# Kernel tuning notes

Hardware: AMD Instinct MI355X
Metric: run time of the kernel (lower is better)

The kernel has to match this reference:

```python
import jax, jax.numpy as jnp
import numpy as np

WINDOW, SIM_TH, GAMMA, L_MAX, NUM_HEADS = 32, 0.7, 0.8, 1024, 8


def setup_inputs() -> dict:
    key = jax.random.key(0)
    ks = jax.random.split(key, 12)
    B, N, F, D, S, V, C = 8, 16384, 1024, 512, 64, 30522, 4
    padded_bags = jax.random.normal(ks[0], (B, N, F), jnp.float32)
    lengths = jax.random.randint(ks[1], (B,), N // 4, N + 1)
    key_padding_mask = jnp.arange(N)[None, :] >= lengths[:, None]  # True = pad (tail)
    input_ids = jax.random.randint(ks[2], (B, S), 0, V)
    attention_mask = jnp.ones((B, S), jnp.int32)

    def xav(k, shape):
        lim = np.sqrt(6.0 / (shape[0] + shape[1]))
        return jax.random.uniform(k, shape, jnp.float32, -lim, lim)

    emb_table = jax.random.normal(ks[3], (V, 768), jnp.float32) * 0.02
    return dict(
        padded_bags=padded_bags, key_padding_mask=key_padding_mask,
        input_ids=input_ids, attention_mask=attention_mask,
        emb_table=emb_table,
        W_tp=xav(ks[4], (768, D)), b_tp=jnp.zeros((D,), jnp.float32),
        W_enc=xav(ks[5], (F, D)), b_enc=jnp.zeros((D,), jnp.float32),
        ln_g=jnp.ones((D,), jnp.float32), ln_b=jnp.zeros((D,), jnp.float32),
        Wq=xav(ks[6], (D, D)), bq=jnp.zeros((D,), jnp.float32),
        Wk=xav(ks[7], (D, D)), bk=jnp.zeros((D,), jnp.float32),
        Wv=xav(ks[8], (D, D)), bv=jnp.zeros((D,), jnp.float32),
        Wo=xav(ks[9], (D, D)), bo=jnp.zeros((D,), jnp.float32),
        W_cls=xav(ks[10], (D, C)), b_cls=jnp.zeros((C,), jnp.float32),
    )


def reference(padded_bags, key_padding_mask, input_ids, attention_mask,
              emb_table, W_tp, b_tp, W_enc, b_enc, ln_g, ln_b,
              Wq, bq, Wk, bk, Wv, bv, Wo, bo, W_cls, b_cls):
    B, N, _ = padded_bags.shape
    D = W_enc.shape[1]
    # --- frozen text encoder surrogate (DistilBERT is frozen + no_grad in original):
    # token embedding + masked mean pooling stands in for the CLS feature [B,768]
    tok = emb_table[input_ids]                                   # [B,S,768]
    am = attention_mask[..., None].astype(jnp.float32)
    text_feat = (tok * am).sum(1) / jnp.maximum(am.sum(1), 1.0)
    text_feat = jax.lax.stop_gradient(text_feat)
    text_emb = text_feat @ W_tp + b_tp                           # [B,D]
    # --- feature encoder: Linear + LayerNorm + ReLU (dropout = eval identity) ---
    h = padded_bags @ W_enc + b_enc                              # [B,N,D]
    mu = h.mean(-1, keepdims=True)
    var = ((h - mu) ** 2).mean(-1, keepdims=True)
    img = jax.nn.relu(ln_g * (h - mu) / jnp.sqrt(var + 1e-5) + ln_b)
    valid = ~key_padding_mask                                    # [B,N]
    # --- Stage 1: sliding-window (size 32) cosine-similarity redundancy pruning ---
    fn = img / (jnp.linalg.norm(img, axis=-1, keepdims=True) + 1e-8)
    neg = jnp.full((B, N), -jnp.inf, jnp.float32)
    max_sim = neg
    for w in range(1, WINDOW + 1):                               # fixed small window loop
        sim_w = (fn[:, w:] * fn[:, :-w]).sum(-1)                 # [B,N-w]
        sim_w = jnp.where(valid[:, :-w], sim_w, -jnp.inf)
        max_sim = jnp.maximum(max_sim, jnp.concatenate([neg[:, :w], sim_w], axis=1))
    keep1 = valid & (max_sim < SIM_TH)                           # [B,N]
    # --- Stage 2: language-guided top-k by text relevance, kept in original order ---
    rel = jnp.einsum('bnd,bd->bn', img, text_emb)
    rel_m = jnp.where(keep1, rel, -jnp.inf)
    n_kept = keep1.sum(-1)
    k_b = jnp.clip((GAMMA * n_kept.astype(jnp.float32)).astype(jnp.int32), 1, L_MAX)
    _, idx = jax.lax.top_k(rel_m, L_MAX)                         # [B,L_MAX]
    sel = jnp.arange(L_MAX)[None, :] < k_b[:, None]
    idx_sorted = jnp.sort(jnp.where(sel, idx, N), axis=-1)       # sort -> original order
    mask2 = idx_sorted < N
    feat2 = jnp.take_along_axis(img, jnp.clip(idx_sorted, 0, N - 1)[..., None], axis=1)
    feat2 = jnp.where(mask2[..., None], feat2, 0.0)              # [B,L_MAX,D] zero-repadded
    # --- Stage 3: sequential visual token compression (adjacent-pair mean pooling) ---
    M = L_MAX // 2
    f2 = feat2.reshape(B, M, 2, D)
    pm = mask2.reshape(B, M, 2).astype(jnp.float32)
    feat3 = (f2 * pm[..., None]).sum(2) / jnp.maximum(pm.sum(2), 1.0)[..., None]  # [B,M,D]
    # --- cross-modal MHA aggregator (text query; zero-padded keys DO attend, as in original) ---
    H = NUM_HEADS
    dh = D // H
    q = (text_emb @ Wq + bq).reshape(B, H, dh)
    k = (feat3 @ Wk + bk).reshape(B, M, H, dh)
    v = (feat3 @ Wv + bv).reshape(B, M, H, dh)
    scores = jnp.einsum('bhd,bmhd->bhm', q, k) / np.float32(np.sqrt(dh))
    attn = jax.nn.softmax(scores, axis=-1)
    ctx = jnp.einsum('bhm,bmhd->bhd', attn, v).reshape(B, D)
    out = ctx @ Wo + bo
    return out @ W_cls + b_cls                                   # [B,num_classes]
```

## Files before the change

kernel.cpp:

```cpp
#include <hip/hip_runtime.h>
#include <hip/hip_bf16.h>
#include <math.h>
#include <stdint.h>

#define B_    8
#define N_    16384
#define F_    1024
#define D_    512
#define S_    64
#define H_    8
#define DH_   64
#define LMAX_ 1024
#define M2_   512
#define WIN_  32
#define NTOK_ (B_ * N_)

typedef __attribute__((ext_vector_type(8)))  short bf16x8;
typedef __attribute__((ext_vector_type(16))) float f32x16;

#define S_OF(r) (((r) >> 1) & 3)

static __device__ __forceinline__ float wred_sum(float v) {
    #pragma unroll
    for (int d = 1; d < 64; d <<= 1) v += __shfl_xor(v, d, 64);
    return v;
}

static __device__ __forceinline__ void bf8_to_f32(uint4 q, float* a) {
    a[0] = __uint_as_float(q.x << 16); a[1] = __uint_as_float(q.x & 0xffff0000u);
    a[2] = __uint_as_float(q.y << 16); a[3] = __uint_as_float(q.y & 0xffff0000u);
    a[4] = __uint_as_float(q.z << 16); a[5] = __uint_as_float(q.z & 0xffff0000u);
    a[6] = __uint_as_float(q.w << 16); a[7] = __uint_as_float(q.w & 0xffff0000u);
}

static __device__ __forceinline__ unsigned short bf16r(float x) {
    unsigned int b = __float_as_uint(x);
    return (unsigned short)((b + 0x7FFFu + ((b >> 16) & 1u)) >> 16);
}

static __device__ __forceinline__ void split_bf(float x, unsigned short& h, unsigned short& l) {
    unsigned int b = __float_as_uint(x);
    unsigned int hb = (b + 0x7FFFu + ((b >> 16) & 1u)) >> 16;
    h = (unsigned short)hb;
    float r = x - __uint_as_float(hb << 16);
    l = bf16r(r);
}

static __device__ __forceinline__ void split8(float4 f0, float4 f1, bf16x8& hi, bf16x8& lo) {
    float xs[8] = { f0.x, f0.y, f0.z, f0.w, f1.x, f1.y, f1.z, f1.w };
    unsigned int hp[4], lp[4];
    #pragma unroll
    for (int i = 0; i < 4; i++) {
        unsigned int b0 = __float_as_uint(xs[2*i]), b1 = __float_as_uint(xs[2*i+1]);
        hp[i] = (b0 >> 16) | (b1 & 0xffff0000u);
        float r0 = xs[2*i]   - __uint_as_float(b0 & 0xffff0000u);
        float r1 = xs[2*i+1] - __uint_as_float(b1 & 0xffff0000u);
        lp[i] = (__float_as_uint(r0) >> 16) | (__float_as_uint(r1) & 0xffff0000u);
    }
    union { uint4 u; bf16x8 v; } a, c;
    a.u = make_uint4(hp[0], hp[1], hp[2], hp[3]);
    c.u = make_uint4(lp[0], lp[1], lp[2], lp[3]);
    hi = a.v; lo = c.v;
}

static __device__ __forceinline__ void gll16(const void* g, void* l) {
    __builtin_amdgcn_global_load_lds(
        (const __attribute__((address_space(1))) unsigned int*)g,
        (__attribute__((address_space(3))) unsigned int*)l, 16, 0, 0);
}

__global__ void k_detect(const unsigned char* mb, int nbytes, int* flag) {
    int found = 0;
    for (int i = blockIdx.x * blockDim.x + threadIdx.x; i < nbytes; i += gridDim.x * blockDim.x)
        if ((i & 3) && mb[i]) found = 1;
    if (found) atomicOr(flag, 1);
}

__global__ void k_valid(const void* maskp, const int* flag, unsigned char* v) {
    int i = blockIdx.x * 256 + threadIdx.x;
    if (i >= NTOK_) return;
    int pad;
    if (*flag) pad = (((const unsigned char*)maskp)[i] != 0);
    else       pad = (((const int*)maskp)[i] != 0);
    v[i] = pad ? 0 : 1;
}

__global__ void k_text_feat(const float* emb, const int* ids, const int* am, float* tf) {
    int b = blockIdx.x;
    __shared__ int   sid[S_];
    __shared__ float sam[S_];
    int t = threadIdx.x;
    if (t < S_) { sid[t] = ids[b * S_ + t]; sam[t] = (float)am[b * S_ + t]; }
    __syncthreads();
    float asum = 0.f;
    for (int s = 0; s < S_; s++) asum += sam[s];
    float denom = fmaxf(asum, 1.0f);
    for (int d = t; d < 768; d += blockDim.x) {
        float acc = 0.f;
        for (int s = 0; s < S_; s++) acc += emb[(long)sid[s] * 768 + d] * sam[s];
        tf[b * 768 + d] = acc / denom;
    }
}

__global__ void k_rowmm(const float* in, const float* W, const float* bias,
                        float* out, int E, int Nn) {
    int b = blockIdx.x, d = threadIdx.x;
    __shared__ float sin[768];
    for (int e = d; e < E; e += blockDim.x) sin[e] = in[b * E + e];
    __syncthreads();
    float acc = bias[d];
    for (int e = 0; e < E; e++) acc = fmaf(sin[e], W[(long)e * Nn + d], acc);
    out[b * Nn + d] = acc;
}

__global__ __launch_bounds__(256) void k_bsplit_sw(const float* __restrict__ W,
                                                   unsigned short* __restrict__ bh,
                                                   unsigned short* __restrict__ bl,
                                                   int E) {
    __shared__ float tile[32][33];
    int e0 = blockIdx.x * 32;
    int d0 = blockIdx.y * 32;
    int t = threadIdx.x;
    int r = t >> 3, c4 = (t & 7) * 4;
    float4 v = *(const float4*)(W + (long)(e0 + r) * D_ + d0 + c4);
    tile[r][c4] = v.x; tile[r][c4 + 1] = v.y; tile[r][c4 + 2] = v.z; tile[r][c4 + 3] = v.w;
    __syncthreads();
    if (t < 128) {
        int c = t & 31, kq = t >> 5;
        int col = d0 + c;
        float xs[8];
        #pragma unroll
        for (int i = 0; i < 8; i++) xs[i] = tile[kq * 8 + i][c];
        unsigned short h[8], l[8];
        #pragma unroll
        for (int i = 0; i < 8; i++) split_bf(xs[i], h[i], l[i]);
        uint4 ph, pl;
        ph.x = h[0] | ((unsigned)h[1] << 16); ph.y = h[2] | ((unsigned)h[3] << 16);
        ph.z = h[4] | ((unsigned)h[5] << 16); ph.w = h[6] | ((unsigned)h[7] << 16);
        pl.x = l[0] | ((unsigned)l[1] << 16); pl.y = l[2] | ((unsigned)l[3] << 16);
        pl.z = l[4] | ((unsigned)l[5] << 16); pl.w = l[6] | ((unsigned)l[7] << 16);
        int Q = (e0 >> 3) + kq;
        int Qo = (Q & ~3) | ((Q & 3) ^ S_OF(col & 7));
        *(uint4*)(bh + (long)col * E + Qo * 8) = ph;
        *(uint4*)(bl + (long)col * E + Qo * 8) = pl;
    }
}

static __device__ __forceinline__ void gemm3_body(const float* __restrict__ A,
                                                  const unsigned short* __restrict__ Bh2,
                                                  const unsigned short* __restrict__ Bl2,
                                                  const float* __restrict__ bias,
                                                  float* __restrict__ C, int K, int wg) {
    __shared__ __align__(16) float ldsA[128][32];
    __shared__ __align__(16) unsigned short ldsB[2][128][32];
    int bn = wg & 3, bm = wg >> 2;
    int tid = threadIdx.x;
    int w = tid >> 6, lane = tid & 63;
    int r32 = lane & 31, kg = lane >> 5;
    int wr = w >> 1, wc = w & 1;
    int s8 = r32 & 7;

    const float* agbase = nullptr;
    const unsigned short* bgbase = nullptr;
    if (w < 2) {
        int rl = lane >> 3, qs = lane & 7;
        agbase = A + (long)(bm * 128 + w * 64 + rl) * K + ((qs ^ rl) * 4);
    } else {
        const unsigned short* plane = (w == 2) ? Bh2 : Bl2;
        int lrow = lane >> 2, lq = lane & 3;
        bgbase = plane + (long)(bn * 128 + lrow) * K + lq * 8;
    }

    f32x16 acc[2][2];
    #pragma unroll
    for (int i = 0; i < 2; i++)
        #pragma unroll
        for (int j = 0; j < 2; j++)
            #pragma unroll
            for (int r = 0; r < 16; r++) acc[i][j][r] = 0.f;

    for (int kt = 0; kt < K; kt += 32) {
        if (w < 2) {
            #pragma unroll
            for (int j = 0; j < 8; j++)
                gll16(agbase + (long)j * 8 * K + kt, &ldsA[w * 64 + j * 8][0]);
        } else {
            #pragma unroll
            for (int j = 0; j < 8; j++)
                gll16(bgbase + (long)j * 16 * K + kt, &ldsB[w - 2][j * 16][0]);
        }
        __syncthreads();
        #pragma unroll
        for (int k2 = 0; k2 < 2; k2++) {
            int qA = k2 * 4 + kg * 2;
            int qs0 = (qA ^ s8) * 4;
            int qs1 = ((qA + 1) ^ s8) * 4;
            bf16x8 a_h[2], a_l[2];
            #pragma unroll
            for (int rf = 0; rf < 2; rf++) {
                int ar = wr * 64 + rf * 32 + r32;
                float4 f0 = *(const float4*)&ldsA[ar][qs0];
                float4 f1 = *(const float4*)&ldsA[ar][qs1];
                split8(f0, f1, a_h[rf], a_l[rf]);
            }
            int qb = k2 * 2 + kg;
            bf16x8 b_h[2], b_l[2];
            #pragma unroll
            for (int cf = 0; cf < 2; cf++) {
                int bc = wc * 64 + cf * 32 + r32;
                int q = (qb ^ S_OF(r32)) * 8;
                b_h[cf] = *(const bf16x8*)&ldsB[0][bc][q];
                b_l[cf] = *(const bf16x8*)&ldsB[1][bc][q];
            }
            #pragma unroll
            for (int rf = 0; rf < 2; rf++)
                #pragma unroll
                for (int cf = 0; cf < 2; cf++) {
                    acc[rf][cf] = __builtin_amdgcn_mfma_f32_32x32x16_bf16(a_h[rf], b_h[cf], acc[rf][cf], 0, 0, 0);
                    acc[rf][cf] = __builtin_amdgcn_mfma_f32_32x32x16_bf16(a_h[rf], b_l[cf], acc[rf][cf], 0, 0, 0);
                    acc[rf][cf] = __builtin_amdgcn_mfma_f32_32x32x16_bf16(a_l[rf], b_h[cf], acc[rf][cf], 0, 0, 0);
                }
        }
        __syncthreads();
    }
    #pragma unroll
    for (int rf = 0; rf < 2; rf++)
        #pragma unroll
        for (int cf = 0; cf < 2; cf++) {
            int col = bn * 128 + wc * 64 + cf * 32 + r32;
            float bv = bias[col];
            #pragma unroll
            for (int r = 0; r < 16; r++) {
                int row = bm * 128 + wr * 64 + rf * 32 + (r & 3) + 8 * (r >> 2) + 4 * kg;
                C[(long)row * D_ + col] = acc[rf][cf][r] + bv;
            }
        }
}

__global__ __launch_bounds__(256) void k_gemm3p(const float* __restrict__ A,
                                                const unsigned short* __restrict__ Bh2,
                                                const unsigned short* __restrict__ Bl2,
                                                const float* __restrict__ bias,
                                                float* __restrict__ C, int K) {
    int bid = blockIdx.x;
    int cpx = gridDim.x >> 3;
    int wg = (bid & 7) * cpx + (bid >> 3);
    gemm3_body(A, Bh2, Bl2, bias, C, K, wg);
}

__global__ __launch_bounds__(256) void k_gemmkv2(const float* __restrict__ A,
                                                 const unsigned short* __restrict__ Kh, const unsigned short* __restrict__ Kl,
                                                 const float* __restrict__ bk2, float* __restrict__ Ck,
                                                 const unsigned short* __restrict__ Vh, const unsigned short* __restrict__ Vl,
                                                 const float* __restrict__ bv2, float* __restrict__ Cv) {
    int which = blockIdx.x & 1;
    int wg = blockIdx.x >> 1;
    if (which)
        gemm3_body(A, Vh, Vl, bv2, Cv, 512, wg);
    else
        gemm3_body(A, Kh, Kl, bk2, Ck, 512, wg);
}

#define GPAD 40
__global__ __launch_bounds__(256, 3) void k_gemm_mfma(const float* __restrict__ A,
                                                      const unsigned short* __restrict__ Bth,
                                                      const unsigned short* __restrict__ Btl,
                                                      const float* __restrict__ bias,
                                                      float* __restrict__ C) {
    __shared__ __align__(16) unsigned short As[2][64][GPAD];
    __shared__ __align__(16) unsigned short Bs[2][256][GPAD];
    int bm = blockIdx.x, bn = blockIdx.y;
    int tid = threadIdx.x;
    int w = tid >> 6, lane = tid & 63;
    int r32 = lane & 31, kg = lane >> 5;
    f32x16 acc[2][2];
    #pragma unroll
    for (int i = 0; i < 2; i++)
        #pragma unroll
        for (int j = 0; j < 2; j++)
            #pragma unroll
            for (int r = 0; r < 16; r++) acc[i][j][r] = 0.f;
    int arow = tid >> 2, aq = tid & 3;
    const float* abase = A + (long)(bm * 64 + arow) * 1024 + aq * 8;
    const unsigned short* bhbase = Bth + (long)(bn * 256 + tid) * 1024;
    const unsigned short* blbase = Btl + (long)(bn * 256 + tid) * 1024;
    float4 pa0 = *(const float4*)abase;
    float4 pa1 = *(const float4*)(abase + 4);
    for (int kt = 0; kt < 1024; kt += 32) {
        {
            float xs[8] = { pa0.x, pa0.y, pa0.z, pa0.w, pa1.x, pa1.y, pa1.z, pa1.w };
            unsigned short h[8], l[8];
            #pragma unroll
            for (int i = 0; i < 8; i++) split_bf(xs[i], h[i], l[i]);
            uint4 ph, pl;
            ph.x = h[0] | ((unsigned)h[1] << 16); ph.y = h[2] | ((unsigned)h[3] << 16);
            ph.z = h[4] | ((unsigned)h[5] << 16); ph.w = h[6] | ((unsigned)h[7] << 16);
            pl.x = l[0] | ((unsigned)l[1] << 16); pl.y = l[2] | ((unsigned)l[3] << 16);
            pl.z = l[4] | ((unsigned)l[5] << 16); pl.w = l[6] | ((unsigned)l[7] << 16);
            *(uint4*)&As[0][arow][aq * 8] = ph;
            *(uint4*)&As[1][arow][aq * 8] = pl;
        }
        {
            const uint4* ph = (const uint4*)(bhbase + kt);
            const uint4* pl = (const uint4*)(blbase + kt);
            #pragma unroll
            for (int q = 0; q < 4; q++) {
                *(uint4*)&Bs[0][tid][q * 8] = ph[q];
                *(uint4*)&Bs[1][tid][q * 8] = pl[q];
            }
        }
        __syncthreads();
        if (kt + 32 < 1024) {
            const float* ap = abase + kt + 32;
            pa0 = *(const float4*)ap;
            pa1 = *(const float4*)(ap + 4);
        }
        #pragma unroll
        for (int k2 = 0; k2 < 2; k2++) {
            int ko = k2 * 16 + kg * 8;
            bf16x8 ah[2], al[2], bh[2], blv[2];
            #pragma unroll
            for (int rf = 0; rf < 2; rf++) {
                ah[rf] = *(const bf16x8*)&As[0][rf * 32 + r32][ko];
                al[rf] = *(const bf16x8*)&As[1][rf * 32 + r32][ko];
            }
            #pragma unroll
            for (int cf = 0; cf < 2; cf++) {
                bh[cf]  = *(const bf16x8*)&Bs[0][w * 64 + cf * 32 + r32][ko];
                blv[cf] = *(const bf16x8*)&Bs[1][w * 64 + cf * 32 + r32][ko];
            }
            #pragma unroll
            for (int rf = 0; rf < 2; rf++)
                #pragma unroll
                for (int cf = 0; cf < 2; cf++) {
                    acc[rf][cf] = __builtin_amdgcn_mfma_f32_32x32x16_bf16(ah[rf], bh[cf],  acc[rf][cf], 0, 0, 0);
                    acc[rf][cf] = __builtin_amdgcn_mfma_f32_32x32x16_bf16(ah[rf], blv[cf], acc[rf][cf], 0, 0, 0);
                    acc[rf][cf] = __builtin_amdgcn_mfma_f32_32x32x16_bf16(al[rf], bh[cf],  acc[rf][cf], 0, 0, 0);
                }
        }
        __syncthreads();
    }
    #pragma unroll
    for (int rf = 0; rf < 2; rf++)
        #pragma unroll
        for (int cf = 0; cf < 2; cf++) {
            int col = bn * 256 + w * 64 + cf * 32 + r32;
            float bv = bias[col];
            #pragma unroll
            for (int r = 0; r < 16; r++) {
                int row = bm * 64 + rf * 32 + (r & 3) + 8 * (r >> 2) + 4 * kg;
                C[(long)row * D_ + col] = acc[rf][cf][r] + bv;
            }
        }
}

__global__ __launch_bounds__(256) void k_bsplit(const float* __restrict__ W,
                                                unsigned short* __restrict__ bh,
                                                unsigned short* __restrict__ bl) {
    __shared__ float tile[32][33];
    int e0 = blockIdx.x * 32;
    int d0 = blockIdx.y * 32;
    int t = threadIdx.x;
    int r = t >> 3;
    int c = (t & 7) * 4;
    float4 v = *(const float4*)(W + (long)(e0 + r) * D_ + d0 + c);
    tile[r][c] = v.x; tile[r][c + 1] = v.y; tile[r][c + 2] = v.z; tile[r][c + 3] = v.w;
    __syncthreads();
    ushort4 h4, l4;
    unsigned short hh, ll;
    float x0 = tile[c + 0][r], x1 = tile[c + 1][r], x2 = tile[c + 2][r], x3 = tile[c + 3][r];
    split_bf(x0, hh, ll); h4.x = hh; l4.x = ll;
    split_bf(x1, hh, ll); h4.y = hh; l4.y = ll;
    split_bf(x2, hh, ll); h4.z = hh; l4.z = ll;
    split_bf(x3, hh, ll); h4.w = hh; l4.w = ll;
    *(ushort4*)(bh + (long)(d0 + r) * 1024 + e0 + c) = h4;
    *(ushort4*)(bl + (long)(d0 + r) * 1024 + e0 + c) = l4;
}

__global__ __launch_bounds__(256) void k_ln(float* h, const float* g, const float* bb,
                                            const float* temb, float* rnorm, float* rel,
                                            unsigned short* fnb, float2* stats, int write_img) {
    int wid = threadIdx.x >> 6, lane = threadIdx.x & 63;
    long row = (long)blockIdx.x * 4 + wid;
    int b = (int)(row >> 14);
    float* hp = h + row * (long)D_;
    int c0 = lane * 4, c1 = 256 + lane * 4;
    float4 x0 = *(float4*)(hp + c0);
    float4 x1 = *(float4*)(hp + c1);
    float x[8] = { x0.x, x0.y, x0.z, x0.w, x1.x, x1.y, x1.z, x1.w };
    float s = 0.f;
    #pragma unroll
    for (int i = 0; i < 8; i++) s += x[i];
    s = wred_sum(s);
    float mu = s * (1.0f / 512.0f);
    float var = 0.f;
    #pragma unroll
    for (int i = 0; i < 8; i++) { float d = x[i] - mu; var += d * d; }
    var = wred_sum(var) * (1.0f / 512.0f);
    float inv = 1.0f / sqrtf(var + 1e-5f);
    float4 g0 = *(const float4*)(g + c0), g1 = *(const float4*)(g + c1);
    float4 b0 = *(const float4*)(bb + c0), b1 = *(const float4*)(bb + c1);
    float gg[8] = { g0.x, g0.y, g0.z, g0.w, g1.x, g1.y, g1.z, g1.w };
    float bbv[8] = { b0.x, b0.y, b0.z, b0.w, b1.x, b1.y, b1.z, b1.w };
    float y[8], sq = 0.f;
    #pragma unroll
    for (int i = 0; i < 8; i++) {
        y[i] = fmaxf(gg[i] * (x[i] - mu) * inv + bbv[i], 0.0f);
        sq += y[i] * y[i];
    }
    if (write_img) {
        float4 o0 = { y[0], y[1], y[2], y[3] }, o1 = { y[4], y[5], y[6], y[7] };
        *(float4*)(hp + c0) = o0;
        *(float4*)(hp + c1) = o1;
    }
    sq = wred_sum(sq);
    float rn = 1.0f / (sqrtf(sq) + 1e-8f);
    if (fnb) {
        ushort4 u0, u1;
        u0.x = bf16r(y[0] * rn); u0.y = bf16r(y[1] * rn);
        u0.z = bf16r(y[2] * rn); u0.w = bf16r(y[3] * rn);
        u1.x = bf16r(y[4] * rn); u1.y = bf16r(y[5] * rn);
        u1.z = bf16r(y[6] * rn); u1.w = bf16r(y[7] * rn);
        *(ushort4*)(fnb + row * D_ + c0) = u0;
        *(ushort4*)(fnb + row * D_ + c1) = u1;
    }
    const float* tp = temb + (long)b * D_;
    float4 t0 = *(const float4*)(tp + c0), t1 = *(const float4*)(tp + c1);
    float tt[8] = { t0.x, t0.y, t0.z, t0.w, t1.x, t1.y, t1.z, t1.w };
    float rl = 0.f;
    #pragma unroll
    for (int i = 0; i < 8; i++) rl = fmaf(y[i], tt[i], rl);
    rl = wred_sum(rl);
    if (lane == 0) { rnorm[row] = rn; rel[row] = rl; stats[row] = make_float2(mu, inv); }
}

__global__ __launch_bounds__(256) void k_simg(const unsigned short* __restrict__ fnb,
                                              const unsigned char* __restrict__ vld,
                                              int* __restrict__ keep) {
    int wid = threadIdx.x >> 6, lane = threadIdx.x & 63;
    int T = (blockIdx.x * 4 + wid) * 32;
    int r32 = lane & 31, kg = lane >> 5;
    int prevok = (T & (N_ - 1)) != 0;
    const unsigned short* arow  = fnb + (long)(T + r32) * D_ + kg * 8;
    const unsigned short* b0row = fnb + (long)((prevok ? T - 32 : T) + r32) * D_ + kg * 8;

    f32x16 g0, g1;
    #pragma unroll
    for (int r = 0; r < 16; r++) { g0[r] = 0.f; g1[r] = 0.f; }
    #pragma unroll 4
    for (int kt = 0; kt < D_; kt += 16) {
        bf16x8 a  = *(const bf16x8*)(arow + kt);
        bf16x8 b0 = *(const bf16x8*)(b0row + kt);
        g0 = __builtin_amdgcn_mfma_f32_32x32x16_bf16(a, b0, g0, 0, 0, 0);
        g1 = __builtin_amdgcn_mfma_f32_32x32x16_bf16(a, a,  g1, 0, 0, 0);
    }
    int okc0 = prevok ? (int)vld[T - 32 + r32] : 0;
    int okc1 = (int)vld[T + r32];
    float ms[16];
    #pragma unroll
    for (int r = 0; r < 16; r++) {
        int i = (r & 3) + 8 * (r >> 2) + 4 * kg;
        float v = -INFINITY;
        if (okc0 && r32 >= i) v = g0[r];
        if (okc1 && r32 < i)  v = fmaxf(v, g1[r]);
        #pragma unroll
        for (int d = 1; d < 32; d <<= 1) v = fmaxf(v, __shfl_xor(v, d, 64));
        ms[r] = v;
    }
    if (r32 == 0) {
        #pragma unroll
        for (int r = 0; r < 16; r++) {
            int i = (r & 3) + 8 * (r >> 2) + 4 * kg;
            int t = T + i;
            keep[t] = (vld[t] && ms[r] < 0.7f) ? 1 : 0;
        }
    }
}

#define CHUNK 28
#define KROWS 60
__global__ __launch_bounds__(256) void k_sim(const float* img, const float* rnorm,
                                             const unsigned char* vld, int* keep) {
    __shared__ __hip_bfloat16 fnbs[KROWS][D_];
    long c0 = (long)blockIdx.x * CHUNK;
    int tid = threadIdx.x;
    for (int idx = tid; idx < KROWS * (D_ / 8); idx += 256) {
        int rr = idx / (D_ / 8);
        int cc = (idx % (D_ / 8)) * 8;
        long grow = c0 - WIN_ + rr;
        if (grow < 0) grow = 0;
        if (grow >= NTOK_) grow = NTOK_ - 1;
        float rn = rnorm[grow];
        const float* p = img + grow * (long)D_ + cc;
        float4 u = *(const float4*)p, w = *(const float4*)(p + 4);
        fnbs[rr][cc + 0] = __float2bfloat16(u.x * rn);
        fnbs[rr][cc + 1] = __float2bfloat16(u.y * rn);
        fnbs[rr][cc + 2] = __float2bfloat16(u.z * rn);
        fnbs[rr][cc + 3] = __float2bfloat16(u.w * rn);
        fnbs[rr][cc + 4] = __float2bfloat16(w.x * rn);
        fnbs[rr][cc + 5] = __float2bfloat16(w.y * rn);
        fnbs[rr][cc + 6] = __float2bfloat16(w.z * rn);
        fnbs[rr][cc + 7] = __float2bfloat16(w.w * rn);
    }
    __syncthreads();
    int wid = tid >> 6, lane = tid & 63;
    for (int ti = 0; ti < 7; ti++) {
        int tloc = wid * 7 + ti;
        long t = c0 + tloc;
        if (t >= NTOK_) continue;
        int lr = WIN_ + tloc;
        int tl = (int)(t & (N_ - 1));
        float a[8];
        bf8_to_f32(*(const uint4*)&fnbs[lr][lane * 8], a);
        int wmax = tl < WIN_ ? tl : WIN_;
        float msim = -INFINITY;
        for (int w = 1; w <= wmax; w++) {
            if (!vld[t - w]) continue;
            float bvv[8];
            bf8_to_f32(*(const uint4*)&fnbs[lr - w][lane * 8], bvv);
            float p = 0.f;
            #pragma unroll
            for (int i = 0; i < 8; i++) p = fmaf(a[i], bvv[i], p);
            p = wred_sum(p);
            msim = fmaxf(msim, p);
        }
        int kp = (vld[t] && (msim < 0.7f)) ? 1 : 0;
        if (lane == 0) keep[t] = kp;
    }
}

static __device__ void scan1024(int* tot, int tid) {
    if (tid < 64) {
        int vals[16], s = 0;
        #pragma unroll
        for (int i = 0; i < 16; i++) vals[i] = tot[tid * 16 + i];
        #pragma unroll
        for (int i = 0; i < 16; i++) { int t = vals[i]; vals[i] = s; s += t; }
        int inc = s;
        #pragma unroll
        for (int d = 1; d < 64; d <<= 1) {
            int v = __shfl_up(inc, d, 64);
            if ((tid & 63) >= d) inc += v;
        }
        int excl = inc - s;
        #pragma unroll
        for (int i = 0; i < 16; i++) tot[tid * 16 + i] = vals[i] + excl;
    }
}

__global__ __launch_bounds__(1024) void k_topk(const float* rel, const int* keep, int* idxo) {
    int b = blockIdx.x, tid = threadIdx.x;
    const float* relb = rel + (long)b * N_;
    const int* keepb  = keep + (long)b * N_;
    __shared__ unsigned int hist[256];
    __shared__ unsigned int suf[256];
    __shared__ int toti[1024];
    __shared__ int wsum[16];
    __shared__ unsigned int s_prefix;
    __shared__ int s_rem, s_k;

    unsigned int key[16];
    int base = tid * 16, nk_local = 0;
    #pragma unroll
    for (int j = 0; j < 16; j++) {
        int i = base + j;
        float r = relb[i];
        int kp = keepb[i];
        unsigned int bits = __float_as_uint(r);
        unsigned int kk = (bits & 0x80000000u) ? ~bits : (bits | 0x80000000u);
        key[j] = kp ? kk : 0u;
        nk_local += kp;
    }
    int nk = nk_local;
    #pragma unroll
    for (int d = 1; d < 64; d <<= 1) nk += __shfl_xor(nk, d, 64);
    if ((tid & 63) == 0) wsum[tid >> 6] = nk;
    __syncthreads();
    if (tid == 0) {
        int n_kept = 0;
        #pragma unroll
        for (int i = 0; i < 16; i++) n_kept += wsum[i];
        int k = (int)(0.8f * (float)n_kept);
        if (k < 1) k = 1; if (k > LMAX_) k = LMAX_;
        s_k = k; s_rem = k; s_prefix = 0u;
    }
    __syncthreads();

    for (int pass = 0; pass < 4; pass++) {
        int shift = 24 - pass * 8;
        unsigned int himask = (pass == 0) ? 0u : (0xFFFFFFFFu << (shift + 8));
        if (tid < 256) hist[tid] = 0u;
        __syncthreads();
        unsigned int pfx = s_prefix;
        int rem = s_rem;
        #pragma unroll
        for (int j = 0; j < 16; j++) {
            unsigned int kk = key[j];
            if ((kk & himask) == (pfx & himask))
                atomicAdd(&hist[(kk >> shift) & 255], 1u);
        }
        __syncthreads();
        if (tid < 256) suf[tid] = hist[tid];
        __syncthreads();
        for (int o = 1; o < 256; o <<= 1) {
            unsigned int v = 0;
            if (tid < 256 && tid + o < 256) v = suf[tid + o];
            __syncthreads();
            if (tid < 256) suf[tid] += v;
            __syncthreads();
        }
        if (tid < 256) {
            unsigned int sv = suf[tid];
            unsigned int nxt = (tid == 255) ? 0u : suf[tid + 1];
            if (sv >= (unsigned int)rem && nxt < (unsigned int)rem) {
                s_prefix = pfx | ((unsigned int)tid << shift);
                s_rem = rem - (int)nxt;
            }
        }
        __syncthreads();
    }
    unsigned int T = s_prefix;
    int tie_need = s_rem, k = s_k;

    int eq[16], gt[16], eqpre[16];
    int locEq = 0;
    #pragma unroll
    for (int j = 0; j < 16; j++) {
        eq[j] = (key[j] == T); gt[j] = (key[j] > T);
        eqpre[j] = locEq; locEq += eq[j];
    }
    toti[tid] = locEq; __syncthreads();
    scan1024(toti, tid); __syncthreads();
    int eqoff = toti[tid];

    int sel[16], spre[16];
    int locS = 0;
    #pragma unroll
    for (int j = 0; j < 16; j++) {
        int rank = eqoff + eqpre[j];
        sel[j] = gt[j] || (eq[j] && rank < tie_need);
        spre[j] = locS; locS += sel[j];
    }
    __syncthreads();
    toti[tid] = locS; __syncthreads();
    scan1024(toti, tid); __syncthreads();
    int soff = toti[tid];
    #pragma unroll
    for (int j = 0; j < 16; j++)
        if (sel[j]) idxo[b * LMAX_ + soff + spre[j]] = base + j;
    for (int p = k + tid; p < LMAX_; p += 1024) idxo[b * LMAX_ + p] = N_;
}

__global__ void k_feat3(const float* img, const float2* stats, const float* lng,
                        const float* lnb, const int* idxo, float* f3, int recompute) {
    int bm = blockIdx.x;
    int b = bm >> 9, m = bm & 511;
    int i0 = idxo[b * LMAX_ + 2 * m], i1 = idxo[b * LMAX_ + 2 * m + 1];
    int c0 = i0 < N_, c1 = i1 < N_;
    float dn = 1.0f / fmaxf((float)(c0 + c1), 1.0f);
    long r0 = (long)b * N_ + (c0 ? i0 : 0);
    long r1 = (long)b * N_ + (c1 ? i1 : 0);
    int d = threadIdx.x * 4;
    float4 v0 = c0 ? *(const float4*)(img + r0 * D_ + d) : make_float4(0.f, 0.f, 0.f, 0.f);
    float4 v1 = c1 ? *(const float4*)(img + r1 * D_ + d) : make_float4(0.f, 0.f, 0.f, 0.f);
    if (recompute) {
        float4 g4 = *(const float4*)(lng + d);
        float4 b4 = *(const float4*)(lnb + d);
        if (c0) {
            float2 st = stats[r0];
            v0.x = fmaxf(g4.x * (v0.x - st.x) * st.y + b4.x, 0.0f);
            v0.y = fmaxf(g4.y * (v0.y - st.x) * st.y + b4.y, 0.0f);
            v0.z = fmaxf(g4.z * (v0.z - st.x) * st.y + b4.z, 0.0f);
            v0.w = fmaxf(g4.w * (v0.w - st.x) * st.y + b4.w, 0.0f);
        }
        if (c1) {
            float2 st = stats[r1];
            v1.x = fmaxf(g4.x * (v1.x - st.x) * st.y + b4.x, 0.0f);
            v1.y = fmaxf(g4.y * (v1.y - st.x) * st.y + b4.y, 0.0f);
            v1.z = fmaxf(g4.z * (v1.z - st.x) * st.y + b4.z, 0.0f);
            v1.w = fmaxf(g4.w * (v1.w - st.x) * st.y + b4.w, 0.0f);
        }
    }
    float4 o;
    o.x = (v0.x + v1.x) * dn; o.y = (v0.y + v1.y) * dn;
    o.z = (v0.z + v1.z) * dn; o.w = (v0.w + v1.w) * dn;
    *(float4*)(f3 + (long)bm * D_ + d) = o;
}

__global__ __launch_bounds__(512) void k_attn(const float* qv, const float* kk,
                                              const float* vv, float* ctx) {
    int bh = blockIdx.x;
    int b = bh >> 3, h = bh & 7;
    __shared__ float qs[DH_];
    __shared__ float sc[M2_];
    __shared__ float red[M2_];
    __shared__ float part[8][DH_];
    int m = threadIdx.x;
    if (m < DH_) qs[m] = qv[b * D_ + h * DH_ + m];
    __syncthreads();
    const float* kp = kk + (long)b * M2_ * D_ + h * DH_;
    float acc = 0.f;
    #pragma unroll
    for (int d = 0; d < DH_; d += 4) {
        float4 kv = *(const float4*)(kp + (long)m * D_ + d);
        acc += qs[d] * kv.x + qs[d + 1] * kv.y + qs[d + 2] * kv.z + qs[d + 3] * kv.w;
    }
    acc *= 0.125f;
    red[m] = acc; __syncthreads();
    for (int o = 256; o > 0; o >>= 1) { if (m < o) red[m] = fmaxf(red[m], red[m + o]); __syncthreads(); }
    float mx = red[0]; __syncthreads();
    float e = expf(acc - mx);
    sc[m] = e; red[m] = e; __syncthreads();
    for (int o = 256; o > 0; o >>= 1) { if (m < o) red[m] += red[m + o]; __syncthreads(); }
    float inv = 1.0f / red[0];
    int g = m >> 6, d = m & 63;
    const float* vp = vv + (long)b * M2_ * D_ + h * DH_ + d;
    float a2 = 0.f;
    #pragma unroll 4
    for (int mm = g * 64; mm < g * 64 + 64; mm++)
        a2 = fmaf(sc[mm], vp[(long)mm * D_], a2);
    part[g][d] = a2; __syncthreads();
    if (m < DH_) {
        float s = 0.f;
        #pragma unroll
        for (int g2 = 0; g2 < 8; g2++) s += part[g2][m];
        ctx[b * D_ + h * DH_ + m] = s * inv;
    }
}

__global__ __launch_bounds__(512) void k_head(const float* ctx, const float* Wo, const float* bo,
                                              const float* Wc, const float* bc,
                                              float* out) {
    int b = blockIdx.x, d = threadIdx.x;
    __shared__ float cl[D_], ol[D_];
    cl[d] = ctx[b * D_ + d]; __syncthreads();
    float acc = bo[d];
    for (int e = 0; e < D_; e++) acc = fmaf(cl[e], Wo[(long)e * D_ + d], acc);
    ol[d] = acc; __syncthreads();
    if (d < 4) {
        float a2 = bc[d];
        for (int e = 0; e < D_; e++) a2 = fmaf(ol[e], Wc[e * 4 + d], a2);
        out[b * 4 + d] = a2;
    }
}

extern "C" void kernel_launch(void* const* d_in, const int* in_sizes, int n_in,
                              void* d_out, int out_size, void* d_ws, size_t ws_size,
                              hipStream_t stream) {
    const float* bags = (const float*)d_in[0];
    const void*  kpm  = d_in[1];
    const int*   ids  = (const int*)d_in[2];
    const int*   am   = (const int*)d_in[3];
    const float* emb  = (const float*)d_in[4];
    const float* Wtp  = (const float*)d_in[5];
    const float* btp  = (const float*)d_in[6];
    const float* Wen  = (const float*)d_in[7];
    const float* ben  = (const float*)d_in[8];
    const float* lng  = (const float*)d_in[9];
    const float* lnb  = (const float*)d_in[10];
    const float* Wq   = (const float*)d_in[11];
    const float* bq   = (const float*)d_in[12];
    const float* Wk   = (const float*)d_in[13];
    const float* bk   = (const float*)d_in[14];
    const float* Wv   = (const float*)d_in[15];
    const float* bv   = (const float*)d_in[16];
    const float* Wo   = (const float*)d_in[17];
    const float* bo   = (const float*)d_in[18];
    const float* Wc   = (const float*)d_in[19];
    const float* bc   = (const float*)d_in[20];

    char* ws = (char*)d_ws;
    size_t o = 0;
    auto alloc = [&](size_t bytes) -> void* {
        void* p = ws + o; o += (bytes + 255) & ~(size_t)255; return p;
    };
    float* img  = (float*)alloc((size_t)NTOK_ * D_ * 4);
    float* rno  = (float*)alloc((size_t)NTOK_ * 4);
    float* rel  = (float*)alloc((size_t)NTOK_ * 4);
    int*   keep = (int*)alloc((size_t)NTOK_ * 4);
    unsigned char* vld = (unsigned char*)alloc(NTOK_);
    float* tf   = (float*)alloc(B_ * 768 * 4);
    float* te   = (float*)alloc(B_ * D_ * 4);
    float* qv   = (float*)alloc(B_ * D_ * 4);
    int*   idxo = (int*)alloc(B_ * LMAX_ * 4);
    float* f3   = (float*)alloc((size_t)B_ * M2_ * D_ * 4);
    float* kkb  = (float*)alloc((size_t)B_ * M2_ * D_ * 4);
    float* vvb  = (float*)alloc((size_t)B_ * M2_ * D_ * 4);
    float* ctx  = (float*)alloc(B_ * D_ * 4);
    int*   flag = (int*)alloc(256);
    float2* stats = (float2*)alloc((size_t)NTOK_ * 8);
    unsigned short* bth = (unsigned short*)alloc((size_t)D_ * F_ * 2);
    unsigned short* btl = (unsigned short*)alloc((size_t)D_ * F_ * 2);
    unsigned short* wkh = (unsigned short*)alloc((size_t)D_ * D_ * 2);
    unsigned short* wkl = (unsigned short*)alloc((size_t)D_ * D_ * 2);
    unsigned short* wvh = (unsigned short*)alloc((size_t)D_ * D_ * 2);
    unsigned short* wvl = (unsigned short*)alloc((size_t)D_ * D_ * 2);

    size_t fnb_need = (size_t)NTOK_ * D_ * 2 + 4096;
    bool newpath = (ws_size > o) && ((ws_size - o) >= fnb_need);
    unsigned short* fnb = nullptr;
    if (newpath) fnb = (unsigned short*)alloc((size_t)NTOK_ * D_ * 2);

    hipMemsetAsync(flag, 0, 4, stream);
    k_detect<<<64, 256, 0, stream>>>((const unsigned char*)kpm, NTOK_, flag);
    k_valid<<<(NTOK_ + 255) / 256, 256, 0, stream>>>(kpm, flag, vld);
    k_text_feat<<<B_, 256, 0, stream>>>(emb, ids, am, tf);
    k_rowmm<<<B_, 512, 0, stream>>>(tf, Wtp, btp, te, 768, 512);
    k_rowmm<<<B_, 512, 0, stream>>>(te, Wq, bq, qv, 512, 512);

    dim3 gw512(D_ / 32, D_ / 32);
    k_bsplit_sw<<<gw512, 256, 0, stream>>>(Wk, wkh, wkl, D_);
    k_bsplit_sw<<<gw512, 256, 0, stream>>>(Wv, wvh, wvl, D_);

    if (newpath) {
        dim3 gw1024(F_ / 32, D_ / 32);
        k_bsplit_sw<<<gw1024, 256, 0, stream>>>(Wen, bth, btl, F_);
        k_gemm3p<<<4096, 256, 0, stream>>>(bags, bth, btl, ben, img, F_);
    } else {
        dim3 gsplit(F_ / 32, D_ / 32);
        k_bsplit<<<gsplit, 256, 0, stream>>>(Wen, bth, btl);
        dim3 g3(NTOK_ / 64, 2);
        k_gemm_mfma<<<g3, 256, 0, stream>>>(bags, bth, btl, ben, img);
    }

    int write_img = newpath ? 0 : 1;
    k_ln<<<NTOK_ / 4, 256, 0, stream>>>(img, lng, lnb, te, rno, rel, fnb, stats, write_img);
    if (fnb) k_simg<<<NTOK_ / 128, 256, 0, stream>>>(fnb, vld, keep);
    else     k_sim<<<(NTOK_ + CHUNK - 1) / CHUNK, 256, 0, stream>>>(img, rno, vld, keep);
    k_topk<<<B_, 1024, 0, stream>>>(rel, keep, idxo);
    k_feat3<<<B_ * M2_, 128, 0, stream>>>(img, stats, lng, lnb, idxo, f3, newpath ? 1 : 0);

    k_gemmkv2<<<256, 256, 0, stream>>>(f3, wkh, wkl, bk, kkb, wvh, wvl, bv, vvb);

    k_attn<<<B_ * H_, 512, 0, stream>>>(qv, kkb, vvb, ctx);
    k_head<<<B_, 512, 0, stream>>>(ctx, Wo, bo, Wc, bc, (float*)d_out);
}
```

Baseline: 879.2 us.

## Fuse small text/weight-split kernels and retile main GEMM warps to 32x128

Merges the text feature, projection and query kernels into one launch and merges three weight bf16-split launches into one grid. It also changes the main encoder GEMM's warp tiling from 2x2 32x32 fragments to one A fragment against four B fragments per warp. Each warp now does one A split per k-step instead of two but reads four B fragments from LDS instead of two. The fusions cut launch overhead, and the retiling changes the LDS traffic and register balance in the dominant GEMM.

New measurement: 776.8 us, median of 2. -11.6%, faster.

```diff
diff --git a/kernel.cpp b/kernel.cpp
--- a/kernel.cpp
+++ b/kernel.cpp
@@ -85,41 +85,45 @@
     v[i] = pad ? 0 : 1;
 }
 
-__global__ void k_text_feat(const float* emb, const int* ids, const int* am, float* tf) {
-    int b = blockIdx.x;
+__global__ __launch_bounds__(512) void k_text(const float* emb, const int* ids, const int* am,
+                                              const float* Wtp, const float* btp,
+                                              const float* Wq, const float* bq,
+                                              float* te, float* qv) {
+    int b = blockIdx.x, t = threadIdx.x;
     __shared__ int   sid[S_];
     __shared__ float sam[S_];
-    int t = threadIdx.x;
+    __shared__ float tfl[768];
+    __shared__ float tel[D_];
     if (t < S_) { sid[t] = ids[b * S_ + t]; sam[t] = (float)am[b * S_ + t]; }
     __syncthreads();
     float asum = 0.f;
     for (int s = 0; s < S_; s++) asum += sam[s];
     float denom = fmaxf(asum, 1.0f);
-    for (int d = t; d < 768; d += blockDim.x) {
+    for (int d = t; d < 768; d += 512) {
         float acc = 0.f;
         for (int s = 0; s < S_; s++) acc += emb[(long)sid[s] * 768 + d] * sam[s];
-        tf[b * 768 + d] = acc / denom;
-    }
-}
-
-__global__ void k_rowmm(const float* in, const float* W, const float* bias,
-                        float* out, int E, int Nn) {
-    int b = blockIdx.x, d = threadIdx.x;
-    __shared__ float sin[768];
-    for (int e = d; e < E; e += blockDim.x) sin[e] = in[b * E + e];
-    __syncthreads();
-    float acc = bias[d];
-    for (int e = 0; e < E; e++) acc = fmaf(sin[e], W[(long)e * Nn + d], acc);
-    out[b * Nn + d] = acc;
-}
-
-__global__ __launch_bounds__(256) void k_bsplit_sw(const float* __restrict__ W,
+        tfl[d] = acc / denom;
+    }
+    __syncthreads();
+    {
+        float acc = btp[t];
+        for (int e = 0; e < 768; e++) acc = fmaf(tfl[e], Wtp[(long)e * D_ + t], acc);
+        tel[t] = acc;
+        te[b * D_ + t] = acc;
+    }
+    __syncthreads();
+    {
+        float acc = bq[t];
+        for (int e = 0; e < D_; e++) acc = fmaf(tel[e], Wq[(long)e * D_ + t], acc);
+        qv[b * D_ + t] = acc;
+    }
+}
+
+static __device__ __forceinline__ void wsplit_body(const float* __restrict__ W,
                                                    unsigned short* __restrict__ bh,
                                                    unsigned short* __restrict__ bl,
-                                                   int E) {
+                                                   int E, int e0, int d0) {
     __shared__ float tile[32][33];
-    int e0 = blockIdx.x * 32;
-    int d0 = blockIdx.y * 32;
     int t = threadIdx.x;
     int r = t >> 3, c4 = (t & 7) * 4;
     float4 v = *(const float4*)(W + (long)(e0 + r) * D_ + d0 + c4);
@@ -143,6 +147,28 @@
         int Qo = (Q & ~3) | ((Q & 3) ^ S_OF(col & 7));
         *(uint4*)(bh + (long)col * E + Qo * 8) = ph;
         *(uint4*)(bl + (long)col * E + Qo * 8) = pl;
+    }
+}
+
+__global__ __launch_bounds__(256) void k_bsplit_sw(const float* __restrict__ W,
+                                                   unsigned short* __restrict__ bh,
+                                                   unsigned short* __restrict__ bl,
+                                                   int E) {
+    wsplit_body(W, bh, bl, E, blockIdx.x * 32, blockIdx.y * 32);
+}
+
+__global__ __launch_bounds__(256) void k_wsplit(const float* Wen, unsigned short* eh, unsigned short* el,
+                                                const float* Wk2, unsigned short* kh, unsigned short* kl,
+                                                const float* Wv2, unsigned short* vh, unsigned short* vl) {
+    int bid = blockIdx.x;
+    if (bid < 512) {
+        wsplit_body(Wen, eh, el, 1024, (bid >> 4) * 32, (bid & 15) * 32);
+    } else if (bid < 768) {
+        int i = bid - 512;
+        wsplit_body(Wk2, kh, kl, 512, (i >> 4) * 32, (i & 15) * 32);
+    } else {
+        int i = bid - 768;
+        wsplit_body(Wv2, vh, vl, 512, (i >> 4) * 32, (i & 15) * 32);
     }
 }
 
@@ -157,7 +183,6 @@
     int tid = threadIdx.x;
     int w = tid >> 6, lane = tid & 63;
     int r32 = lane & 31, kg = lane >> 5;
-    int wr = w >> 1, wc = w & 1;
     int s8 = r32 & 7;
 
     const float* agbase = nullptr;
@@ -171,13 +196,13 @@
         bgbase = plane + (long)(bn * 128 + lrow) * K + lq * 8;
     }
 
-    f32x16 acc[2][2];
-    #pragma unroll
-    for (int i = 0; i < 2; i++)
-        #pragma unroll
-        for (int j = 0; j < 2; j++)
-            #pragma unroll
-            for (int r = 0; r < 16; r++) acc[i][j][r] = 0.f;
+    f32x16 acc[4];
+    #pragma unroll
+    for (int j = 0; j < 4; j++)
+        #pragma unroll
+        for (int r = 0; r < 16; r++) acc[j][r] = 0.f;
+
+    int ar = w * 32 + r32;
 
     for (int kt = 0; kt < K; kt += 32) {
         if (w < 2) {
@@ -195,46 +220,40 @@
             int qA = k2 * 4 + kg * 2;
             int qs0 = (qA ^ s8) * 4;
             int qs1 = ((qA + 1) ^ s8) * 4;
-            bf16x8 a_h[2], a_l[2];
-            #pragma unroll
-            for (int rf = 0; rf < 2; rf++) {
-                int ar = wr * 64 + rf * 32 + r32;
+            bf16x8 a_h, a_l;
+            {
                 float4 f0 = *(const float4*)&ldsA[ar][qs0];
                 float4 f1 = *(const float4*)&ldsA[ar][qs1];
-                split8(f0, f1, a_h[rf], a_l[rf]);
+                split8(f0, f1, a_h, a_l);
             }
             int qb = k2 * 2 + kg;
-            bf16x8 b_h[2], b_l[2];
-            #pragma unroll
-            for (int cf = 0; cf < 2; cf++) {
-                int bc = wc * 64 + cf * 32 + r32;
-                int q = (qb ^ S_OF(r32)) * 8;
+            int q = (qb ^ S_OF(r32)) * 8;
+            bf16x8 b_h[4], b_l[4];
+            #pragma unroll
+            for (int cf = 0; cf < 4; cf++) {
+                int bc = cf * 32 + r32;
                 b_h[cf] = *(const bf16x8*)&ldsB[0][bc][q];
                 b_l[cf] = *(const bf16x8*)&ldsB[1][bc][q];
             }
             #pragma unroll
-            for (int rf = 0; rf < 2; rf++)
-                #pragma unroll
-                for (int cf = 0; cf < 2; cf++) {
-                    acc[rf][cf] = __builtin_amdgcn_mfma_f32_32x32x16_bf16(a_h[rf], b_h[cf], acc[rf][cf], 0, 0, 0);
-                    acc[rf][cf] = __builtin_amdgcn_mfma_f32_32x32x16_bf16(a_h[rf], b_l[cf], acc[rf][cf], 0, 0, 0);
-                    acc[rf][cf] = __builtin_amdgcn_mfma_f32_32x32x16_bf16(a_l[rf], b_h[cf], acc[rf][cf], 0, 0, 0);
-                }
+            for (int cf = 0; cf < 4; cf++) {
+                acc[cf] = __builtin_amdgcn_mfma_f32_32x32x16_bf16(a_h, b_h[cf], acc[cf], 0, 0, 0);
+                acc[cf] = __builtin_amdgcn_mfma_f32_32x32x16_bf16(a_h, b_l[cf], acc[cf], 0, 0, 0);
+                acc[cf] = __builtin_amdgcn_mfma_f32_32x32x16_bf16(a_l, b_h[cf], acc[cf], 0, 0, 0);
+            }
         }
         __syncthreads();
     }
     #pragma unroll
-    for (int rf = 0; rf < 2; rf++)
-        #pragma unroll
-        for (int cf = 0; cf < 2; cf++) {
-            int col = bn * 128 + wc * 64 + cf * 32 + r32;
-            float bv = bias[col];
-            #pragma unroll
-            for (int r = 0; r < 16; r++) {
-                int row = bm * 128 + wr * 64 + rf * 32 + (r & 3) + 8 * (r >> 2) + 4 * kg;
-                C[(long)row * D_ + col] = acc[rf][cf][r] + bv;
-            }
-        }
+    for (int cf = 0; cf < 4; cf++) {
+        int col = bn * 128 + cf * 32 + r32;
+        float bv = bias[col];
+        #pragma unroll
+        for (int r = 0; r < 16; r++) {
+            int row = bm * 128 + w * 32 + (r & 3) + 8 * (r >> 2) + 4 * kg;
+            C[(long)row * D_ + col] = acc[cf][r] + bv;
+        }
+    }
 }
 
 __global__ __launch_bounds__(256) void k_gemm3p(const float* __restrict__ A,
@@ -779,7 +798,6 @@
     float* rel  = (float*)alloc((size_t)NTOK_ * 4);
     int*   keep = (int*)alloc((size_t)NTOK_ * 4);
     unsigned char* vld = (unsigned char*)alloc(NTOK_);
-    float* tf   = (float*)alloc(B_ * 768 * 4);
     float* te   = (float*)alloc(B_ * D_ * 4);
     float* qv   = (float*)alloc(B_ * D_ * 4);
     int*   idxo = (int*)alloc(B_ * LMAX_ * 4);
@@ -804,19 +822,15 @@
     hipMemsetAsync(flag, 0, 4, stream);
     k_detect<<<64, 256, 0, stream>>>((const unsigned char*)kpm, NTOK_, flag);
     k_valid<<<(NTOK_ + 255) / 256, 256, 0, stream>>>(kpm, flag, vld);
-    k_text_feat<<<B_, 256, 0, stream>>>(emb, ids, am, tf);
-    k_rowmm<<<B_, 512, 0, stream>>>(tf, Wtp, btp, te, 768, 512);
-    k_rowmm<<<B_, 512, 0, stream>>>(te, Wq, bq, qv, 512, 512);
-
-    dim3 gw512(D_ / 32, D_ / 32);
-    k_bsplit_sw<<<gw512, 256, 0, stream>>>(Wk, wkh, wkl, D_);
-    k_bsplit_sw<<<gw512, 256, 0, stream>>>(Wv, wvh, wvl, D_);
+    k_text<<<B_, 512, 0, stream>>>(emb, ids, am, Wtp, btp, Wq, bq, te, qv);
 
     if (newpath) {
-        dim3 gw1024(F_ / 32, D_ / 32);
-        k_bsplit_sw<<<gw1024, 256, 0, stream>>>(Wen, bth, btl, F_);
+        k_wsplit<<<1024, 256, 0, stream>>>(Wen, bth, btl, Wk, wkh, wkl, Wv, wvh, wvl);
         k_gemm3p<<<4096, 256, 0, stream>>>(bags, bth, btl, ben, img, F_);
     } else {
+        dim3 gw512(D_ / 32, D_ / 32);
+        k_bsplit_sw<<<gw512, 256, 0, stream>>>(Wk, wkh, wkl, D_);
+        k_bsplit_sw<<<gw512, 256, 0, stream>>>(Wv, wvh, wvl, D_);
         dim3 gsplit(F_ / 32, D_ / 32);
         k_bsplit<<<gsplit, 256, 0, stream>>>(Wen, bth, btl);
         dim3 g3(NTOK_ / 64, 2);
```
